# Kernel tuning notes

Measured on AMD Instinct MI355X. Metric: run time of the kernel, lower is better.

The kernel has to match this reference:

```python
import jax, jax.numpy as jnp
import numpy as np

B, T, D = 2, 1024, 2048
H = 16
NOPE, ROPE = 128, 64
QKD = NOPE + ROPE          # 192
QLORA, KVLORA = 1536, 512
VHD = 128
INTER = 8192
EPS = 1e-6
# NOTE: faithful to source: softscale = qk_head_dim * -0.5 (a large negative
# multiplier, NOT qk_head_dim ** -0.5). We reproduce the exact math.
SOFTSCALE = QKD * -0.5


def rmsnorm(x, w):
    return x * jax.lax.rsqrt(jnp.mean(jnp.square(x), axis=-1, keepdims=True) + EPS) * w


def apply_rope(x, cos, sin):
    # x: [B, T, h, rd] with rd even; cos/sin: [T, rd//2]
    x2 = x.reshape(x.shape[:-1] + (-1, 2))
    x0, x1 = x2[..., 0], x2[..., 1]
    c = cos[None, :, None, :]
    s = sin[None, :, None, :]
    r0 = x0 * c - x1 * s
    r1 = x0 * s + x1 * c
    return jnp.stack([r0, r1], axis=-1).reshape(x.shape)


def setup_inputs() -> dict:
    key = jax.random.key(0)
    ks = jax.random.split(key, 12)

    def w(k, o, i):
        return jax.random.normal(k, (o, i), jnp.float32) * 0.02

    x = jax.random.normal(ks[0], (B, T, D), jnp.float32)
    # RoPE angle tables for the rope sub-dim
    inv_freq = 1.0 / (10000.0 ** (jnp.arange(0, ROPE, 2, dtype=jnp.float32) / ROPE))
    ang = jnp.arange(T, dtype=jnp.float32)[:, None] * inv_freq[None, :]  # [T, ROPE//2]
    # causal additive mask [T, T]
    mask = jnp.where(jnp.tril(jnp.ones((T, T), bool)), 0.0, -1e9).astype(jnp.float32)
    return {
        "x": x,
        "mask": mask,
        "freqs_cos": jnp.cos(ang),
        "freqs_sin": jnp.sin(ang),
        "attn_norm_w": jnp.ones((D,), jnp.float32),
        "wq_a": w(ks[1], QLORA, D),
        "q_norm_w": jnp.ones((QLORA,), jnp.float32),
        "wq_b": w(ks[2], H * QKD, QLORA),
        "wkv_a": w(ks[3], KVLORA + ROPE, D),
        "kv_norm_w": jnp.ones((KVLORA,), jnp.float32),
        "wkv_b": w(ks[4], H * (NOPE + VHD), KVLORA),
        "wo": w(ks[5], D, H * VHD),
        "ffn_norm_w": jnp.ones((D,), jnp.float32),
        "w1": w(ks[6], INTER, D),
        "w2": w(ks[7], D, INTER),
        "w3": w(ks[8], INTER, D),
    }


def reference(x, mask, freqs_cos, freqs_sin, attn_norm_w, wq_a, q_norm_w, wq_b,
              wkv_a, kv_norm_w, wkv_b, wo, ffn_norm_w, w1, w2, w3):
    b, t, d = x.shape
    # --- MLA attention sub-block (pre-norm + residual) ---
    h = rmsnorm(x, attn_norm_w)
    # low-rank query: wq_b(q_norm(wq_a(h)))
    q = rmsnorm(h @ wq_a.T, q_norm_w) @ wq_b.T          # [b, t, H*QKD]
    q = q.reshape(b, t, H, QKD)
    q_nope, q_pe = q[..., :NOPE], q[..., NOPE:]
    q_pe = apply_rope(q_pe, freqs_cos, freqs_sin)
    # low-rank kv + decoupled rope key
    kv_all = h @ wkv_a.T                                 # [b, t, KVLORA+ROPE]
    kv_lat, k_pe = kv_all[..., :KVLORA], kv_all[..., KVLORA:]
    k_pe = apply_rope(k_pe[:, :, None, :], freqs_cos, freqs_sin)  # [b, t, 1, ROPE]
    kv = rmsnorm(kv_lat, kv_norm_w) @ wkv_b.T            # [b, t, H*(NOPE+VHD)]
    kv = kv.reshape(b, t, H, NOPE + VHD)
    k_nope, v = kv[..., :NOPE], kv[..., NOPE:]
    qf = jnp.concatenate([q_nope, q_pe], axis=-1)        # [b, t, H, QKD]
    kf = jnp.concatenate([k_nope, jnp.broadcast_to(k_pe, (b, t, H, ROPE))], axis=-1)
    scores = jnp.einsum('bshd,bthd->bsht', qf, kf) * SOFTSCALE
    scores = scores + mask[:, None, :]                   # mask over (s, 1, t)
    attn = jax.nn.softmax(scores.astype(jnp.float32), axis=-1).astype(x.dtype)
    y = jnp.einsum('bsht,bthd->bshd', attn, v).reshape(b, t, H * VHD)
    x = x + y @ wo.T
    # --- MLP sub-block (pre-norm + residual), SwiGLU ---
    h2 = rmsnorm(x, ffn_norm_w)
    out = x + (jax.nn.silu(h2 @ w1.T) * (h2 @ w3.T)) @ w2.T
    return out
```

## Files before the change

kernel.cpp:

```cpp
#include <hip/hip_runtime.h>
#include <hip/hip_bf16.h>
#include <cstddef>


#define TT 1024
#define DD 2048
#define QBLK 64
#define KVB 32

using bf16 = __hip_bfloat16;
typedef __attribute__((ext_vector_type(8))) short short8;
typedef __attribute__((ext_vector_type(8))) unsigned short ushort8v;
typedef __attribute__((ext_vector_type(4))) float f32x4;

__device__ __forceinline__ float us2f(unsigned short u) {
    return __uint_as_float(((unsigned int)u) << 16);
}
__device__ __forceinline__ float ldf(const void* p, size_t i, int isbf) {
    return isbf ? us2f(((const unsigned short*)p)[i]) : ((const float*)p)[i];
}
__device__ __forceinline__ unsigned short f2bf(float f) {
    __hip_bfloat16 b = __float2bfloat16(f);
    return *reinterpret_cast<unsigned short*>(&b);
}
// ... 58 lines not shown
            for (int u = 0; u < 8; ++u) {
                const float v = s[u];
                th[u] = f2bf(v);
                tl[u] = f2bf(v - us2f(th[u]));
            }
        }
        *(ushort8v*)(dh + i) = *(const ushort8v*)th;
        *(ushort8v*)(dl + i) = *(const ushort8v*)tl;
    }
}

template <int S, int HASR>
__global__ __launch_bounds__(256) void combine_k(
    const float* __restrict__ p, const float* __restrict__ R,
    float* __restrict__ out, int n4)
{
    const int stride = gridDim.x * 256;
    const float4* pp = (const float4*)p;
    for (int i = blockIdx.x * 256 + threadIdx.x; i < n4; i += stride) {
        float4 o = pp[i];
#pragma unroll
        for (int s = 1; s < S; ++s) {
            const float4 b4 = pp[(size_t)s * n4 + i];
            o.x += b4.x; o.y += b4.y; o.z += b4.z; o.w += b4.w;
        }
        if (HASR) {
            const float4 r4 = ((const float4*)R)[i];
            o.x += r4.x; o.y += r4.y; o.z += r4.z; o.w += r4.w;
        }
        ((float4*)out)[i] = o;
    }
}

__global__ __launch_bounds__(256) void rmsnorm_hl_k(
    const float* __restrict__ in, const void* __restrict__ w,
    unsigned short* __restrict__ oh, unsigned short* __restrict__ ol,
    int L, int istride, const int* __restrict__ flag)
{
    const int isbf = *flag;
    const int m = blockIdx.x, tid = threadIdx.x;
    const float* row = in + (size_t)m * istride;
    float ss = 0.f;
    for (int i = tid; i < L; i += 256) { float v = row[i]; ss += v * v; }
    __shared__ float red[256];
    red[tid] = ss; __syncthreads();
    for (int s = 128; s > 0; s >>= 1) {
        if (tid < s) red[tid] += red[tid + s];
        __syncthreads();
    }
    const float scale = 1.0f / sqrtf(red[0] / (float)L + 1e-6f);
    unsigned short* hrow = oh + (size_t)m * L;
    unsigned short* lrow = ol + (size_t)m * L;
    for (int i = tid; i < L; i += 256) {
        const float v = row[i] * scale * ldf(w, i, isbf);
        const unsigned short hi = f2bf(v);
        hrow[i] = hi;
        lrow[i] = f2bf(v - us2f(hi));
    }
}

__global__ __launch_bounds__(256) void rmsnorm_bf_k(
    const float* __restrict__ in, const void* __restrict__ w,
    unsigned short* __restrict__ out, int L,
    const int* __restrict__ flag)
{
    const int isbf = *flag;
    const int m = blockIdx.x, tid = threadIdx.x;
    const float* row = in + (size_t)m * L;
    float ss = 0.f;
    for (int i = tid; i < L; i += 256) { float v = row[i]; ss += v * v; }
    __shared__ float red[256];
    red[tid] = ss; __syncthreads();
    for (int s = 128; s > 0; s >>= 1) {
        if (tid < s) red[tid] += red[tid + s];
        __syncthreads();
    }
    const float scale = 1.0f / sqrtf(red[0] / (float)L + 1e-6f);
    unsigned short* orow = out + (size_t)m * L;
    for (int i = tid; i < L; i += 256)
        orow[i] = f2bf(row[i] * scale * ldf(w, i, isbf));
}

__global__ __launch_bounds__(256) void rmsnorm_x_hl_k(
    const void* __restrict__ x, size_t eoff, const void* __restrict__ w,
    unsigned short* __restrict__ hh, unsigned short* __restrict__ hl,
    float* __restrict__ xf, const int* __restrict__ flag)
{
    const int isbf = *flag;
    const int m = blockIdx.x, tid = threadIdx.x;
    const size_t base = eoff + (size_t)m * DD;
    float* xrow = xf + (size_t)m * DD;
    float ss = 0.f;
    float vals[8];
    for (int i = 0; i < 8; ++i) {
        float v = ldf(x, base + tid + 256 * i, isbf);
        vals[i] = v; ss += v * v;
        xrow[tid + 256 * i] = v;
    }
    __shared__ float red[256];
    red[tid] = ss; __syncthreads();
    for (int s = 128; s > 0; s >>= 1) {
        if (tid < s) red[tid] += red[tid + s];
        __syncthreads();
    }
    const float scale = 1.0f / sqrtf(red[0] / (float)DD + 1e-6f);
    unsigned short* hrow = hh + (size_t)m * DD;
    unsigned short* lrow = hl + (size_t)m * DD;
    for (int i = 0; i < 8; ++i) {
        const float v = vals[i] * scale * ldf(w, tid + 256 * i, isbf);
        const unsigned short hi = f2bf(v);
        hrow[tid + 256 * i] = hi;
        lrow[tid + 256 * i] = f2bf(v - us2f(hi));
    }
}

__global__ __launch_bounds__(256) void gemm_mfma3_k(
    const unsigned short* __restrict__ Ah, const unsigned short* __restrict__ Al,
    const void* __restrict__ Wv, const unsigned short* __restrict__ Wlo,
    float* __restrict__ C, int N, int K, int klen,
    int presplit, const int* __restrict__ flag)
{
    __shared__ __align__(16) unsigned short lds[20480];
    const int tid = threadIdx.x;
    const int lane = tid & 63;
    const int wave = tid >> 6;
    const int wm = (wave >> 1) << 6, wn = (wave & 1) << 6;
    const int bm = blockIdx.y << 7, bn = blockIdx.x << 7;
    const int k0 = blockIdx.z * klen;
    const size_t zoff = (size_t)blockIdx.z * 1024 * N;
    const int frow = lane & 15;
    const int fk = (lane >> 4) << 3;
    const int kend = k0 + klen;

    f32x4 acc[4][4] = {};

    if (presplit) {
        unsigned short* Lah = lds;
        unsigned short* Lal = lds + 4096;
        unsigned short* Lwh = lds + 8192;
        unsigned short* Lwl = lds + 12288;
        const unsigned short* Whp = (const unsigned short*)Wv;
        const int lrow = lane >> 2;
        const int sp8 = ((lane & 3) ^ (lrow & 3)) << 3;
        const int rA0 = wave * 32 + lrow;
        const int rA1 = wave * 32 + 16 + lrow;
        const int wr0 = (bn + rA0 < N) ? bn + rA0 : N - 1;
        const int wr1 = (bn + rA1 < N) ? bn + rA1 : N - 1;
        const size_t gA0 = (size_t)(bm + rA0) * K + sp8;
        const size_t gA1 = (size_t)(bm + rA1) * K + sp8;
        const size_t gW0 = (size_t)wr0 * K + sp8;
        const size_t gW1 = (size_t)wr1 * K + sp8;
        unsigned short* d0 = lds + wave * 1024;
        const int xa = ((fk >> 3) ^ (frow & 3)) << 3;

        for (int kt = k0; kt < kend; kt += 32) {
            gld16(Ah + gA0 + kt, Lah + wave * 1024);
            gld16(Ah + gA1 + kt, Lah + wave * 1024 + 512);
            gld16(Al + gA0 + kt, Lal + wave * 1024);
            gld16(Al + gA1 + kt, Lal + wave * 1024 + 512);
            gld16(Whp + gW0 + kt, Lwh + wave * 1024);
            gld16(Whp + gW1 + kt, Lwh + wave * 1024 + 512);
            gld16(Wlo + gW0 + kt, Lwl + wave * 1024);
            gld16(Wlo + gW1 + kt, Lwl + wave * 1024 + 512);
            __syncthreads();

            short8 afh[4], afl[4], bfh[4], bfl[4];
#pragma unroll
            for (int i = 0; i < 4; ++i) {
                afh[i] = *(const short8*)&Lah[(wm + i * 16 + frow) * 32 + xa];
                afl[i] = *(const short8*)&Lal[(wm + i * 16 + frow) * 32 + xa];
            }
#pragma unroll
            for (int j = 0; j < 4; ++j) {
                bfh[j] = *(const short8*)&Lwh[(wn + j * 16 + frow) * 32 + xa];
                bfl[j] = *(const short8*)&Lwl[(wn + j * 16 + frow) * 32 + xa];
            }
#pragma unroll
            for (int i = 0; i < 4; ++i)
#pragma unroll
                for (int j = 0; j < 4; ++j) {
                    acc[i][j] = __builtin_amdgcn_mfma_f32_16x16x32_bf16(
                        afh[i], bfh[j], acc[i][j], 0, 0, 0);
                    acc[i][j] = __builtin_amdgcn_mfma_f32_16x16x32_bf16(
                        afh[i], bfl[j], acc[i][j], 0, 0, 0);
                    acc[i][j] = __builtin_amdgcn_mfma_f32_16x16x32_bf16(
                        afl[i], bfh[j], acc[i][j], 0, 0, 0);
                }
            __syncthreads();
        }
        (void)d0;
    } else {
        unsigned short* Ash = lds;
        unsigned short* Asl = lds + 5120;
        unsigned short* Wsh = lds + 10240;
        unsigned short* Wsl = lds + 15360;
        const int isbf = *flag;
        const int srow = tid >> 1, scol = (tid & 1) << 4;
        const unsigned short* Ahld = Ah + (size_t)(bm + srow) * K + scol;
        const unsigned short* Alld = Al + (size_t)(bm + srow) * K + scol;
        const int wrow = bn + srow;
        const size_t wldbase = (size_t)((wrow < N) ? wrow : (N - 1)) * K + scol;
        unsigned short* Ahdst = &Ash[srow * 40 + scol];
        unsigned short* Aldst = &Asl[srow * 40 + scol];
        unsigned short* Whdst = &Wsh[srow * 40 + scol];
        unsigned short* Wldst = &Wsl[srow * 40 + scol];
        for (int kt = k0; kt < kend; kt += 32) {
            ushort8v a0h = *(const ushort8v*)(Ahld + kt);
            ushort8v a1h = *(const ushort8v*)(Ahld + kt + 8);
            ushort8v a0l = *(const ushort8v*)(Alld + kt);
            ushort8v a1l = *(const ushort8v*)(Alld + kt + 8);
            ushort8v w0h, w1h, w0l, w1l;
            if (isbf) {
                const unsigned short* Wp = (const unsigned short*)Wv + wldbase + kt;
                w0h = *(const ushort8v*)(Wp);
                w1h = *(const ushort8v*)(Wp + 8);
                w0l = w0h ^ w0h;
                w1l = w0l;
            } else {
                const float* Wp = (const float*)Wv + wldbase + kt;
                unsigned short th[16], tl[16];
#pragma unroll
                for (int t4 = 0; t4 < 4; ++t4) {
                    float4 f = *(const float4*)(Wp + 4 * t4);
                    float fv[4] = {f.x, f.y, f.z, f.w};
#pragma unroll
                    for (int u = 0; u < 4; ++u) {
                        const unsigned short hi = f2bf(fv[u]);
                        th[4 * t4 + u] = hi;
                        tl[4 * t4 + u] = f2bf(fv[u] - us2f(hi));
                    }
                }
                w0h = *(ushort8v*)&th[0]; w1h = *(ushort8v*)&th[8];
                w0l = *(ushort8v*)&tl[0]; w1l = *(ushort8v*)&tl[8];
            }
            __syncthreads();
            *(ushort8v*)Ahdst = a0h; *(ushort8v*)(Ahdst + 8) = a1h;
            *(ushort8v*)Aldst = a0l; *(ushort8v*)(Aldst + 8) = a1l;
            *(ushort8v*)Whdst = w0h; *(ushort8v*)(Whdst + 8) = w1h;
            *(ushort8v*)Wldst = w0l; *(ushort8v*)(Wldst + 8) = w1l;
            __syncthreads();

            short8 afh[4], afl[4], bfh[4], bfl[4];
#pragma unroll
            for (int i = 0; i < 4; ++i) {
                afh[i] = *(const short8*)&Ash[(wm + i * 16 + frow) * 40 + fk];
                afl[i] = *(const short8*)&Asl[(wm + i * 16 + frow) * 40 + fk];
            }
#pragma unroll
            for (int j = 0; j < 4; ++j) {
                bfh[j] = *(const short8*)&Wsh[(wn + j * 16 + frow) * 40 + fk];
                bfl[j] = *(const short8*)&Wsl[(wn + j * 16 + frow) * 40 + fk];
            }
#pragma unroll
            for (int i = 0; i < 4; ++i)
#pragma unroll
                for (int j = 0; j < 4; ++j) {
                    acc[i][j] = __builtin_amdgcn_mfma_f32_16x16x32_bf16(
                        afh[i], bfh[j], acc[i][j], 0, 0, 0);
                    acc[i][j] = __builtin_amdgcn_mfma_f32_16x16x32_bf16(
                        afh[i], bfl[j], acc[i][j], 0, 0, 0);
                    acc[i][j] = __builtin_amdgcn_mfma_f32_16x16x32_bf16(
                        afl[i], bfh[j], acc[i][j], 0, 0, 0);
                }
        }
    }

#pragma unroll
    for (int i = 0; i < 4; ++i) {
        const int r0 = bm + wm + i * 16 + ((lane >> 4) << 2);
#pragma unroll
        for (int j = 0; j < 4; ++j) {
            const int c = bn + wn + j * 16 + (lane & 15);
            if (c < N) {
#pragma unroll
                for (int g = 0; g < 4; ++g)
                    C[zoff + (size_t)(r0 + g) * N + c] = acc[i][j][g];
            }
        }
    }
}

template <int EPI>
__global__ __launch_bounds__(256) void gemm_mfma_k(
    const unsigned short* __restrict__ A, const void* __restrict__ Wv,
    const float* __restrict__ R, void* __restrict__ outp,
    int N, int K, int klen, int wready, const int* __restrict__ flag)
{
    __shared__ __align__(16) unsigned short lds[10240];
    const int tid = threadIdx.x;
    const int lane = tid & 63;
    const int wave = tid >> 6;
    const int wm = (wave >> 1) << 6, wn = (wave & 1) << 6;
    const int bm = blockIdx.y << 7, bn = blockIdx.x << 7;
    const int k0 = blockIdx.z * klen;
    const size_t zoff = (size_t)blockIdx.z * 1024 * N;
    const int frow = lane & 15;
    const int fk = (lane >> 4) << 3;
    const int kend = k0 + klen;

    f32x4 acc[4][4] = {};

    if (wready) {
        unsigned short* As = lds;
        unsigned short* Ws = lds + 4096;
        const unsigned short* Wp = (const unsigned short*)Wv;
        const int lrow = lane >> 2;
        const int sp8 = ((lane & 3) ^ (lrow & 3)) << 3;
        const int rA0 = wave * 32 + lrow;
        const int rA1 = wave * 32 + 16 + lrow;
        const size_t gA0 = (size_t)(bm + rA0) * K + sp8;
        const size_t gA1 = (size_t)(bm + rA1) * K + sp8;
        const size_t gW0 = (size_t)(bn + rA0) * K + sp8;
        const size_t gW1 = (size_t)(bn + rA1) * K + sp8;
        const int xa = ((fk >> 3) ^ (frow & 3)) << 3;

        for (int kt = k0; kt < kend; kt += 32) {
            gld16(A + gA0 + kt, As + wave * 1024);
            gld16(A + gA1 + kt, As + wave * 1024 + 512);
            gld16(Wp + gW0 + kt, Ws + wave * 1024);
            gld16(Wp + gW1 + kt, Ws + wave * 1024 + 512);
            __syncthreads();

            short8 af[4], bfr[4];
#pragma unroll
            for (int i = 0; i < 4; ++i)
                af[i] = *(const short8*)&As[(wm + i * 16 + frow) * 32 + xa];
#pragma unroll
            for (int j = 0; j < 4; ++j)
                bfr[j] = *(const short8*)&Ws[(wn + j * 16 + frow) * 32 + xa];
#pragma unroll
            for (int i = 0; i < 4; ++i)
#pragma unroll
                for (int j = 0; j < 4; ++j)
                    acc[i][j] = __builtin_amdgcn_mfma_f32_16x16x32_bf16(
                        af[i], bfr[j], acc[i][j], 0, 0, 0);
            __syncthreads();
        }
    } else {
        unsigned short* As = lds;
        unsigned short* Ws = lds + 5120;
        const int isbf = *flag;
        const int srow = tid >> 1, scol = (tid & 1) << 4;
        const unsigned short* Ald = A + (size_t)(bm + srow) * K + scol;
        const size_t wldbase = (size_t)(bn + srow) * K + scol;
        unsigned short* Adst = &As[srow * 40 + scol];
        unsigned short* Wdst = &Ws[srow * 40 + scol];
        for (int kt = k0; kt < kend; kt += 32) {
            ushort8v a0 = *(const ushort8v*)(Ald + kt);
            ushort8v a1 = *(const ushort8v*)(Ald + kt + 8);
            ushort8v w0, w1;
            if (isbf) {
                const unsigned short* Wpp = (const unsigned short*)Wv + wldbase + kt;
                w0 = *(const ushort8v*)(Wpp);
                w1 = *(const ushort8v*)(Wpp + 8);
            } else {
                const float* Wpp = (const float*)Wv + wldbase + kt;
                float4 f0 = *(const float4*)(Wpp);
                float4 f1 = *(const float4*)(Wpp + 4);
                float4 f2 = *(const float4*)(Wpp + 8);
                float4 f3 = *(const float4*)(Wpp + 12);
                unsigned short wt[16];
                wt[0] = f2bf(f0.x); wt[1] = f2bf(f0.y); wt[2]  = f2bf(f0.z); wt[3]  = f2bf(f0.w);
                wt[4] = f2bf(f1.x); wt[5] = f2bf(f1.y); wt[6]  = f2bf(f1.z); wt[7]  = f2bf(f1.w);
                wt[8] = f2bf(f2.x); wt[9] = f2bf(f2.y); wt[10] = f2bf(f2.z); wt[11] = f2bf(f2.w);
                wt[12] = f2bf(f3.x); wt[13] = f2bf(f3.y); wt[14] = f2bf(f3.z); wt[15] = f2bf(f3.w);
                w0 = *(const ushort8v*)&wt[0];
                w1 = *(const ushort8v*)&wt[8];
            }
            __syncthreads();
            *(ushort8v*)Adst = a0; *(ushort8v*)(Adst + 8) = a1;
            *(ushort8v*)Wdst = w0; *(ushort8v*)(Wdst + 8) = w1;
            __syncthreads();

            short8 af[4], bfr[4];
#pragma unroll
            for (int i = 0; i < 4; ++i)
                af[i] = *(const short8*)&As[(wm + i * 16 + frow) * 40 + fk];
#pragma unroll
// ... 98 lines not shown
        unsigned short* As = lds;
        unsigned short* Ws1 = lds + 5120;
        unsigned short* Ws3 = lds + 10240;
        const int isbf = *flag;
        const int srow = tid >> 1, scol = (tid & 1) << 4;
        const unsigned short* Ald = A + (size_t)(bm + srow) * K + scol;
        const size_t wldbase = (size_t)(bn + srow) * K + scol;
        unsigned short* Adst = &As[srow * 40 + scol];
        unsigned short* W1dst = &Ws1[srow * 40 + scol];
        unsigned short* W3dst = &Ws3[srow * 40 + scol];
        for (int kt = 0; kt < K; kt += 32) {
            ushort8v a0 = *(const ushort8v*)(Ald + kt);
            ushort8v a1 = *(const ushort8v*)(Ald + kt + 8);
            ushort8v w10, w11, w30, w31;
            if (isbf) {
                const unsigned short* W1p = (const unsigned short*)W1v + wldbase + kt;
                const unsigned short* W3p = (const unsigned short*)W3v + wldbase + kt;
                w10 = *(const ushort8v*)(W1p); w11 = *(const ushort8v*)(W1p + 8);
                w30 = *(const ushort8v*)(W3p); w31 = *(const ushort8v*)(W3p + 8);
            } else {
                const float* W1p = (const float*)W1v + wldbase + kt;
                const float* W3p = (const float*)W3v + wldbase + kt;
                unsigned short t1[16], t3[16];
#pragma unroll
                for (int t4 = 0; t4 < 4; ++t4) {
                    float4 f1 = *(const float4*)(W1p + 4 * t4);
                    float4 f3 = *(const float4*)(W3p + 4 * t4);
                    float v1[4] = {f1.x, f1.y, f1.z, f1.w};
                    float v3[4] = {f3.x, f3.y, f3.z, f3.w};
#pragma unroll
                    for (int u = 0; u < 4; ++u) {
                        t1[4 * t4 + u] = f2bf(v1[u]);
                        t3[4 * t4 + u] = f2bf(v3[u]);
                    }
                }
                w10 = *(ushort8v*)&t1[0]; w11 = *(ushort8v*)&t1[8];
                w30 = *(ushort8v*)&t3[0]; w31 = *(ushort8v*)&t3[8];
            }
            __syncthreads();
            *(ushort8v*)Adst = a0; *(ushort8v*)(Adst + 8) = a1;
            *(ushort8v*)W1dst = w10; *(ushort8v*)(W1dst + 8) = w11;
            *(ushort8v*)W3dst = w30; *(ushort8v*)(W3dst + 8) = w31;
            __syncthreads();

            short8 af[4], b1[4], b3[4];
#pragma unroll
            for (int i = 0; i < 4; ++i)
                af[i] = *(const short8*)&As[(wm + i * 16 + frow) * 40 + fk];
#pragma unroll
            for (int j = 0; j < 4; ++j) {
                b1[j] = *(const short8*)&Ws1[(wn + j * 16 + frow) * 40 + fk];
                b3[j] = *(const short8*)&Ws3[(wn + j * 16 + frow) * 40 + fk];
            }
#pragma unroll
            for (int i = 0; i < 4; ++i)
#pragma unroll
                for (int j = 0; j < 4; ++j) {
                    acc1[i][j] = __builtin_amdgcn_mfma_f32_16x16x32_bf16(
                        af[i], b1[j], acc1[i][j], 0, 0, 0);
                    acc3[i][j] = __builtin_amdgcn_mfma_f32_16x16x32_bf16(
                        af[i], b3[j], acc3[i][j], 0, 0, 0);
                }
        }
    }

#pragma unroll
    for (int i = 0; i < 4; ++i) {
        const int r0 = bm + wm + i * 16 + ((lane >> 4) << 2);
#pragma unroll
        for (int j = 0; j < 4; ++j) {
            const int c = bn + wn + j * 16 + (lane & 15);
#pragma unroll
            for (int g = 0; g < 4; ++g) {
                const float gv = acc1[i][j][g];
                const float sg = 1.0f / (1.0f + __expf(-gv));
                outp[(size_t)(r0 + g) * N + c] = f2bf(gv * sg * acc3[i][j][g]);
            }
        }
    }
}

__global__ __launch_bounds__(256) void rope_k(
    float* __restrict__ qb, float* __restrict__ kva,
    const void* __restrict__ fc, const void* __restrict__ fs,
    const int* __restrict__ flag)
{
    const int isbf = *flag;
    const int t = blockIdx.x;
    const int tid = threadIdx.x;
    __shared__ float c[32], s[32];
    if (tid < 32) {
        c[tid] = ldf(fc, t * 32 + tid, isbf);
        s[tid] = ldf(fs, t * 32 + tid, isbf);
    }
    __syncthreads();
    for (int p = tid; p < 512; p += 256) {
        const int h = p >> 5, i = p & 31;
        float* base = qb + (size_t)t * 3072 + h * 192 + 128 + 2 * i;
        const float x0 = base[0], x1 = base[1];
        base[0] = x0 * c[i] - x1 * s[i];
        base[1] = x0 * s[i] + x1 * c[i];
    }
    if (tid < 32) {
        float* base = kva + (size_t)t * 576 + 512 + 2 * tid;
        const float x0 = base[0], x1 = base[1];
        base[0] = x0 * c[tid] - x1 * s[tid];
        base[1] = x0 * s[tid] + x1 * c[tid];
    }
}

__global__ __launch_bounds__(256) void kvprep_k(
    const float* __restrict__ kvb,
    const float* __restrict__ kva,
    unsigned short* __restrict__ kh, unsigned short* __restrict__ kl,
    unsigned short* __restrict__ vt)
{
    const int tt = blockIdx.x, h = blockIdx.y;
    const int tid = threadIdx.x;
    const int tbase = tt * 64;
    for (int i = tid; i < 64 * 192; i += 256) {
        const int t = i / 192, k = i % 192;
        const float v = (k < 128)
            ? kvb[(size_t)(tbase + t) * 4096 + h * 256 + k]
            : kva[(size_t)(tbase + t) * 576 + 512 + (k - 128)];
        const unsigned short hi = f2bf(v);
        const size_t o = ((size_t)h * 1024 + tbase + t) * 192 + k;
        kh[o] = hi;
        kl[o] = f2bf(v - us2f(hi));
    }
    __shared__ unsigned short Vl[128][72];
    for (int i = tid; i < 64 * 128; i += 256) {
        const int t = i >> 7, d = i & 127;
        Vl[d][t] = f2bf(kvb[(size_t)(tbase + t) * 4096 + h * 256 + 128 + d]);
    }
    __syncthreads();
    for (int i = tid; i < 128 * 64; i += 256) {
        const int d = i >> 6, t = i & 63;
        vt[((size_t)h * 128 + d) * 1024 + tbase + t] = Vl[d][t];
    }
}

__global__ __launch_bounds__(256) void attn_mfma_k(
    const float* __restrict__ qb,
    const unsigned short* __restrict__ kh,
    const unsigned short* __restrict__ kl,
    const unsigned short* __restrict__ vt,
    float* __restrict__ opart)
{
    const int qt = blockIdx.x, h = blockIdx.y, z = blockIdx.z;
    const int s0 = qt * QBLK;
    const int tid = threadIdx.x;
    const int lane = tid & 63, wave = tid >> 6;
    const int frow = lane & 15;
    const int fk8 = (lane >> 4) << 3;
    const int g4 = (lane >> 4) << 2;

    __shared__ __align__(16) unsigned short Ksh[KVB][200];
    __shared__ __align__(16) unsigned short Ksl[KVB][200];
    __shared__ __align__(16) unsigned short Vs[128][40];
    __shared__ __align__(16) unsigned short Ps[4][16][40];

    const int wrow0 = s0 + wave * 16;
    short8 qhf[6], qlf[6];
    {
        const float* qrow = qb + (size_t)(wrow0 + frow) * 3072 + h * 192 + fk8;
#pragma unroll
        for (int ks = 0; ks < 6; ++ks) {
            float4 f0 = *(const float4*)(qrow + ks * 32);
            float4 f1 = *(const float4*)(qrow + ks * 32 + 4);
            float fv[8] = {f0.x, f0.y, f0.z, f0.w, f1.x, f1.y, f1.z, f1.w};
            unsigned short th[8], tl[8];
#pragma unroll
            for (int u = 0; u < 8; ++u) {
                th[u] = f2bf(fv[u]);
                tl[u] = f2bf(fv[u] - us2f(th[u]));
            }
            qhf[ks] = *(short8*)th;
            qlf[ks] = *(short8*)tl;
        }
    }

    f32x4 O[8] = {};
    float m_run[4] = {-1e30f, -1e30f, -1e30f, -1e30f};
    float l_run[4] = {};

    const int t_beg = z * (qt + 1);
    const int t_end = t_beg + (qt + 1);
    for (int tt = t_beg; tt < t_end; ++tt) {
        const int t0 = tt * KVB;
        __syncthreads();
        for (int i = tid; i < KVB * 24; i += 256) {
            const int r = i / 24, c = (i % 24) * 8;
            const size_t gof = ((size_t)h * 1024 + t0 + r) * 192 + c;
            *(ushort8v*)&Ksh[r][c] = *(const ushort8v*)(kh + gof);
            *(ushort8v*)&Ksl[r][c] = *(const ushort8v*)(kl + gof);
        }
        for (int i = tid; i < 128 * 4; i += 256) {
            const int d = i >> 2, c = (i & 3) * 8;
            *(ushort8v*)&Vs[d][c] =
                *(const ushort8v*)(vt + ((size_t)h * 128 + d) * 1024 + t0 + c);
        }
        __syncthreads();

        const bool active = (t0 <= wrow0 + 15);
        if (active) {
            f32x4 s[2] = {};
#pragma unroll
            for (int j = 0; j < 2; ++j) {
                const unsigned short* kb = &Ksh[j * 16 + frow][fk8];
                const unsigned short* lb = &Ksl[j * 16 + frow][fk8];
#pragma unroll
                for (int ks = 0; ks < 6; ++ks) {
                    short8 bh = *(const short8*)(kb + ks * 32);
                    short8 bl = *(const short8*)(lb + ks * 32);
                    s[j] = __builtin_amdgcn_mfma_f32_16x16x32_bf16(qhf[ks], bh, s[j], 0, 0, 0);
                    s[j] = __builtin_amdgcn_mfma_f32_16x16x32_bf16(qhf[ks], bl, s[j], 0, 0, 0);
                    s[j] = __builtin_amdgcn_mfma_f32_16x16x32_bf16(qlf[ks], bh, s[j], 0, 0, 0);
                }
            }
            const bool edge = (t0 + KVB - 1 > wrow0);
            float sv[2][4];
#pragma unroll
            for (int j = 0; j < 2; ++j)
#pragma unroll
                for (int g = 0; g < 4; ++g) {
                    float v = s[j][g] * -96.0f;
                    if (edge) {
                        const int col = t0 + j * 16 + frow;
                        const int row = wrow0 + g4 + g;
                        if (col > row) v = -1e30f;
                    }
                    sv[j][g] = v;
                }
            float alpha[4];
#pragma unroll
            for (int g = 0; g < 4; ++g) {
                float mt = fmaxf(sv[0][g], sv[1][g]);
                mt = fmaxf(mt, __shfl_xor(mt, 1));
                mt = fmaxf(mt, __shfl_xor(mt, 2));
                mt = fmaxf(mt, __shfl_xor(mt, 4));
                mt = fmaxf(mt, __shfl_xor(mt, 8));
                const float mn = fmaxf(m_run[g], mt);
                alpha[g] = __expf(m_run[g] - mn);
                m_run[g] = mn;
                const float p0 = __expf(sv[0][g] - mn);
                const float p1 = __expf(sv[1][g] - mn);
                sv[0][g] = p0; sv[1][g] = p1;
                float ps = p0 + p1;
                ps += __shfl_xor(ps, 1);
                ps += __shfl_xor(ps, 2);
                ps += __shfl_xor(ps, 4);
                ps += __shfl_xor(ps, 8);
                l_run[g] = l_run[g] * alpha[g] + ps;
            }
#pragma unroll
            for (int jt = 0; jt < 8; ++jt)
#pragma unroll
                for (int g = 0; g < 4; ++g)
                    O[jt][g] *= alpha[g];
#pragma unroll
            for (int j = 0; j < 2; ++j)
#pragma unroll
                for (int g = 0; g < 4; ++g)
                    Ps[wave][g4 + g][j * 16 + frow] = f2bf(sv[j][g]);
        }
        __syncthreads();
        if (active) {
            short8 pa = *(const short8*)&Ps[wave][frow][fk8];
#pragma unroll
            for (int jt = 0; jt < 8; ++jt) {
                short8 vb = *(const short8*)&Vs[jt * 16 + frow][fk8];
                O[jt] = __builtin_amdgcn_mfma_f32_16x16x32_bf16(pa, vb, O[jt], 0, 0, 0);
            }
        }
    }

#pragma unroll
    for (int g = 0; g < 4; ++g) {
        const int row = wrow0 + g4 + g;
        float* rec = opart + (((size_t)z * 1024 + row) * 16 + h) * 66;
        unsigned short* ob = (unsigned short*)rec;
#pragma unroll
        for (int jt = 0; jt < 8; ++jt)
            ob[jt * 16 + frow] = f2bf(O[jt][g]);
        if ((lane & 15) == 0) { rec[64] = m_run[g]; rec[65] = l_run[g]; }
    }
}

__global__ __launch_bounds__(256) void attn_merge_k(
    const float* __restrict__ opart, unsigned short* __restrict__ y)
{
    const int r = blockIdx.x;
    for (int i = threadIdx.x; i < 2048; i += 256) {
        const int h = i >> 7, d = i & 127;
        const float* r0 = opart + (((size_t)r) * 16 + h) * 66;
        const float* r1 = opart + (((size_t)1024 + r) * 16 + h) * 66;
        const float m0 = r0[64], l0 = r0[65];
        const float m1 = r1[64], l1 = r1[65];
        const float mm = fmaxf(m0, m1);
        const float a0 = __expf(m0 - mm), a1 = __expf(m1 - mm);
        const float denom = l0 * a0 + l1 * a1;
        const float o0 = us2f(((const unsigned short*)r0)[d]);
        const float o1 = us2f(((const unsigned short*)r1)[d]);
        y[(size_t)r * 2048 + h * 128 + d] = f2bf((o0 * a0 + o1 * a1) / denom);
    }
}

extern "C" void kernel_launch(void* const* d_in, const int* in_sizes, int n_in,
                              void* d_out, int out_size, void* d_ws, size_t ws_size,
                              hipStream_t stream) {
    (void)in_sizes; (void)n_in; (void)out_size;
    const void* x       = d_in[0];
    const void* fcos    = d_in[2];
    const void* fsin    = d_in[3];
    const void* attn_nw = d_in[4];
    const void* wq_a    = d_in[5];
    const void* q_nw    = d_in[6];
    const void* wq_b    = d_in[7];
    const void* wkv_a   = d_in[8];
    const void* kv_nw   = d_in[9];
    const void* wkv_b   = d_in[10];
    const void* wo      = d_in[11];
    const void* ffn_nw  = d_in[12];
    const void* w1      = d_in[13];
    const void* w2      = d_in[14];
    const void* w3      = d_in[15];

    int* flag = (int*)d_ws;
    float* a  = (float*)d_ws + 64;
    const size_t M1 = 1048576;
    float* xf  = a;
    unsigned short* hh = (unsigned short*)(a + 2 * M1);
    unsigned short* hl = (unsigned short*)(a + 3 * M1);
    float* qa  = a + 4 * M1;
    float* kva = a + 4 * M1;
    unsigned short* kvnh = (unsigned short*)(a + 4 * M1 + 655360);
    unsigned short* kvnl = (unsigned short*)(a + 4 * M1 + 655360 + 262144);
    unsigned short* qah = (unsigned short*)(a + 5 * M1 + 524288);
    unsigned short* qal = (unsigned short*)(a + 6 * M1 + 262144);
    float* qb  = a + 7 * M1;
    float* kvb = a + 10 * M1;
    unsigned short* kh = (unsigned short*)(a + 2 * M1);
    unsigned short* kl = (unsigned short*)(a + 5 * M1 + 524288);
    unsigned short* vt = (unsigned short*)(a + 14 * M1);
    unsigned short* yb = (unsigned short*)(a + 3 * M1 + 524288);
    unsigned short* hb  = (unsigned short*)(a + 2 * M1);
    unsigned short* gb2 = (unsigned short*)(a + 12 * M1);
    float* x2  = xf;
    float* sp  = a + 10 * M1;
    float* fpo = a + 5 * M1;
    float* fp2 = a + 2 * M1;
    float* opart = a + 10 * M1;
    unsigned short* wo_b  = (unsigned short*)(a + 16 * M1);
    unsigned short* w1_b  = (unsigned short*)(a + 18 * M1);
    unsigned short* w3_b  = (unsigned short*)(a + 26 * M1);
    unsigned short* w2_b  = (unsigned short*)(a + 34 * M1);
    unsigned short* wqa_h = (unsigned short*)(a + 42 * M1);
    unsigned short* wqa_l = wqa_h + 3145728u;
    unsigned short* wqb_h = (unsigned short*)(a + 45 * M1);
    unsigned short* wqb_l = wqb_h + 4718592u;
    unsigned short* wkva_h = (unsigned short*)(a + 49 * M1 + 524288);
    unsigned short* wkva_l = wkva_h + 1179648u;
    unsigned short* wkvb_h = (unsigned short*)(a + 50 * M1 + 655360);
    unsigned short* wkvb_l = wkvb_h + 2097152u;
    const size_t NEED = 256 + (size_t)(52 * M1 + 655360) * 4;
    const int prep = (ws_size >= NEED) ? 1 : 0;

    detect_k<<<1, 64, 0, stream>>>(x, flag);

    if (prep) {
        cvt_bf_k<<<1024, 256, 0, stream>>>(wo, wo_b, (size_t)2048 * 2048, flag);
        cvt_bf_k<<<2048, 256, 0, stream>>>(w1, w1_b, (size_t)8192 * 2048, flag);
        cvt_bf_k<<<2048, 256, 0, stream>>>(w3, w3_b, (size_t)8192 * 2048, flag);
        cvt_bf_k<<<2048, 256, 0, stream>>>(w2, w2_b, (size_t)2048 * 8192, flag);
        cvt_hl_k<<<1024, 256, 0, stream>>>(wq_a, wqa_h, wqa_l, (size_t)1536 * 2048, flag);
        cvt_hl_k<<<1024, 256, 0, stream>>>(wq_b, wqb_h, wqb_l, (size_t)3072 * 1536, flag);
        cvt_hl_k<<<512, 256, 0, stream>>>(wkv_a, wkva_h, wkva_l, (size_t)576 * 2048, flag);
        cvt_hl_k<<<1024, 256, 0, stream>>>(wkv_b, wkvb_h, wkvb_l, (size_t)4096 * 512, flag);
    }
    const void* Wqa = prep ? (const void*)wqa_h : wq_a;
    const void* Wqb = prep ? (const void*)wqb_h : wq_b;
    const void* Wkva = prep ? (const void*)wkva_h : wkv_a;
    const void* Wkvb = prep ? (const void*)wkvb_h : wkv_b;
    const unsigned short* WqaL = prep ? wqa_l : nullptr;
    const unsigned short* WqbL = prep ? wqb_l : nullptr;
    const unsigned short* WkvaL = prep ? wkva_l : nullptr;
    const unsigned short* WkvbL = prep ? wkvb_l : nullptr;
    const void* WoP = prep ? (const void*)wo_b : wo;
    const void* W1P = prep ? (const void*)w1_b : w1;
    const void* W3P = prep ? (const void*)w3_b : w3;
    const void* W2P = prep ? (const void*)w2_b : w2;

    for (int b = 0; b < 2; ++b) {
        const size_t eoff = (size_t)b * TT * DD;
        float* outb = (float*)d_out + eoff;

        rmsnorm_x_hl_k<<<TT, 256, 0, stream>>>(x, eoff, attn_nw, hh, hl, xf, flag);
        gemm_mfma3_k<<<dim3(12, 8, 4), 256, 0, stream>>>(hh, hl, Wqa, WqaL, sp, 1536, 2048, 512, prep, flag);
        combine_k<4, 0><<<1024, 256, 0, stream>>>(sp, nullptr, qa, 393216);
        rmsnorm_hl_k<<<TT, 256, 0, stream>>>(qa, q_nw, qah, qal, 1536, 1536, flag);
        gemm_mfma3_k<<<dim3(24, 8, 2), 256, 0, stream>>>(qah, qal, Wqb, WqbL, sp, 3072, 1536, 768, prep, flag);
        combine_k<2, 0><<<1024, 256, 0, stream>>>(sp, nullptr, qb, 786432);
        gemm_mfma3_k<<<dim3(5, 8, 8), 256, 0, stream>>>(hh, hl, Wkva, WkvaL, sp, 576, 2048, 256, prep, flag);
        combine_k<8, 0><<<1024, 256, 0, stream>>>(sp, nullptr, kva, 147456);
        rmsnorm_hl_k<<<TT, 256, 0, stream>>>(kva, kv_nw, kvnh, kvnl, 512, 576, flag);
        rope_k<<<TT, 256, 0, stream>>>(qb, kva, fcos, fsin, flag);
        gemm_mfma3_k<<<dim3(32, 8, 1), 256, 0, stream>>>(kvnh, kvnl, Wkvb, WkvbL, kvb, 4096, 512, 512, prep, flag);
        kvprep_k<<<dim3(16, 16), 256, 0, stream>>>(kvb, kva, kh, kl, vt);
        attn_mfma_k<<<dim3(TT / QBLK, 16, 2), 256, 0, stream>>>(qb, kh, kl, vt, opart);
        attn_merge_k<<<TT, 256, 0, stream>>>(opart, yb);

        gemm_mfma_k<0><<<dim3(16, 8, 4), 256, 0, stream>>>(yb, WoP, nullptr, fpo, 2048, 2048, 512, prep, flag);
        combine_k<4, 1><<<1024, 256, 0, stream>>>(fpo, xf, x2, 524288);
        rmsnorm_bf_k<<<TT, 256, 0, stream>>>(x2, ffn_nw, hb, 2048, flag);
        gemm_swiglu_k<<<dim3(64, 8), 256, 0, stream>>>(hb, W1P, W3P, gb2, 8192, 2048, prep, flag);
        gemm_mfma_k<0><<<dim3(16, 8, 4), 256, 0, stream>>>(gb2, W2P, nullptr, fp2, 2048, 8192, 2048, prep, flag);
        combine_k<4, 1><<<1024, 256, 0, stream>>>(fp2, x2, outb, 524288);
    }
}
```

Measured before the change: 1.325 ms.

## Process both batches in one launch sequence and fuse KV prep into GEMM epilogue

```diff
diff --git a/kernel.cpp b/kernel.cpp
--- a/kernel.cpp
+++ b/kernel.cpp
@@ -164,13 +164,13 @@
 }
 
 __global__ __launch_bounds__(256) void rmsnorm_x_hl_k(
-    const void* __restrict__ x, size_t eoff, const void* __restrict__ w,
+    const void* __restrict__ x, const void* __restrict__ w,
     unsigned short* __restrict__ hh, unsigned short* __restrict__ hl,
     float* __restrict__ xf, const int* __restrict__ flag)
 {
     const int isbf = *flag;
     const int m = blockIdx.x, tid = threadIdx.x;
-    const size_t base = eoff + (size_t)m * DD;
+    const size_t base = (size_t)m * DD;
     float* xrow = xf + (size_t)m * DD;
     float ss = 0.f;
     float vals[8];
@@ -200,7 +200,9 @@
     const unsigned short* __restrict__ Ah, const unsigned short* __restrict__ Al,
     const void* __restrict__ Wv, const unsigned short* __restrict__ Wlo,
     float* __restrict__ C, int N, int K, int klen,
-    int presplit, const int* __restrict__ flag)
+    int presplit, const int* __restrict__ flag,
+    int epikv, unsigned short* __restrict__ okh,
+    unsigned short* __restrict__ okl, unsigned short* __restrict__ ovt)
 {
     __shared__ __align__(16) unsigned short lds[20480];
     const int tid = threadIdx.x;
@@ -209,7 +211,7 @@
     const int wm = (wave >> 1) << 6, wn = (wave & 1) << 6;
     const int bm = blockIdx.y << 7, bn = blockIdx.x << 7;
     const int k0 = blockIdx.z * klen;
-    const size_t zoff = (size_t)blockIdx.z * 1024 * N;
+    const size_t zoff = (size_t)blockIdx.z * 2048 * N;
     const int frow = lane & 15;
     const int fk = (lane >> 4) << 3;
     const int kend = k0 + klen;
@@ -232,7 +234,6 @@
         const size_t gA1 = (size_t)(bm + rA1) * K + sp8;
         const size_t gW0 = (size_t)wr0 * K + sp8;
         const size_t gW1 = (size_t)wr1 * K + sp8;
-        unsigned short* d0 = lds + wave * 1024;
         const int xa = ((fk >> 3) ^ (frow & 3)) << 3;
 
         for (int kt = k0; kt < kend; kt += 32) {
@@ -270,7 +271,6 @@
                 }
             __syncthreads();
         }
-        (void)d0;
     } else {
         unsigned short* Ash = lds;
         unsigned short* Asl = lds + 5120;
@@ -347,16 +347,41 @@
         }
     }
 
-#pragma unroll
-    for (int i = 0; i < 4; ++i) {
-        const int r0 = bm + wm + i * 16 + ((lane >> 4) << 2);
-#pragma unroll
-        for (int j = 0; j < 4; ++j) {
-            const int c = bn + wn + j * 16 + (lane & 15);
-            if (c < N) {
-#pragma unroll
-                for (int g = 0; g < 4; ++g)
-                    C[zoff + (size_t)(r0 + g) * N + c] = acc[i][j][g];
+    if (!epikv) {
+#pragma unroll
+        for (int i = 0; i < 4; ++i) {
+            const int r0 = bm + wm + i * 16 + ((lane >> 4) << 2);
+#pragma unroll
+            for (int j = 0; j < 4; ++j) {
+                const int c = bn + wn + j * 16 + (lane & 15);
+                if (c < N) {
+#pragma unroll
+                    for (int g = 0; g < 4; ++g)
+                        C[zoff + (size_t)(r0 + g) * N + c] = acc[i][j][g];
+                }
+            }
+        }
+    } else {
+#pragma unroll
+        for (int i = 0; i < 4; ++i) {
+            const int r0 = bm + wm + i * 16 + ((lane >> 4) << 2);
+#pragma unroll
+            for (int j = 0; j < 4; ++j) {
+                const int c = bn + wn + j * 16 + (lane & 15);
+                const int h = c >> 8, cc = c & 255;
+#pragma unroll
+                for (int g = 0; g < 4; ++g) {
+                    const int t = r0 + g;
+                    const float v = acc[i][j][g];
+                    if (cc < 128) {
+                        const size_t o = ((size_t)h * 2048 + t) * 192 + cc;
+                        const unsigned short hi = f2bf(v);
+                        okh[o] = hi;
+                        okl[o] = f2bf(v - us2f(hi));
+                    } else {
+                        ovt[((size_t)h * 128 + (cc - 128)) * 2048 + t] = f2bf(v);
+                    }
+                }
             }
         }
     }
@@ -375,7 +400,7 @@
     const int wm = (wave >> 1) << 6, wn = (wave & 1) << 6;
     const int bm = blockIdx.y << 7, bn = blockIdx.x << 7;
     const int k0 = blockIdx.z * klen;
-    const size_t zoff = (size_t)blockIdx.z * 1024 * N;
+    const size_t zoff = (size_t)blockIdx.z * 2048 * N;
     const int frow = lane & 15;
     const int fk = (lane >> 4) << 3;
     const int kend = k0 + klen;
@@ -640,11 +665,13 @@
 
 __global__ __launch_bounds__(256) void rope_k(
     float* __restrict__ qb, float* __restrict__ kva,
+    unsigned short* __restrict__ kh, unsigned short* __restrict__ kl,
     const void* __restrict__ fc, const void* __restrict__ fs,
     const int* __restrict__ flag)
 {
     const int isbf = *flag;
-    const int t = blockIdx.x;
+    const int r = blockIdx.x;
+    const int t = r & 1023;
     const int tid = threadIdx.x;
     __shared__ float c[32], s[32];
     if (tid < 32) {
@@ -654,47 +681,26 @@
     __syncthreads();
     for (int p = tid; p < 512; p += 256) {
         const int h = p >> 5, i = p & 31;
-        float* base = qb + (size_t)t * 3072 + h * 192 + 128 + 2 * i;
+        float* base = qb + (size_t)r * 3072 + h * 192 + 128 + 2 * i;
         const float x0 = base[0], x1 = base[1];
         base[0] = x0 * c[i] - x1 * s[i];
         base[1] = x0 * s[i] + x1 * c[i];
     }
     if (tid < 32) {
-        float* base = kva + (size_t)t * 576 + 512 + 2 * tid;
+        float* base = kva + (size_t)r * 576 + 512 + 2 * tid;
         const float x0 = base[0], x1 = base[1];
-        base[0] = x0 * c[tid] - x1 * s[tid];
-        base[1] = x0 * s[tid] + x1 * c[tid];
-    }
-}
-
-__global__ __launch_bounds__(256) void kvprep_k(
-    const float* __restrict__ kvb,
-    const float* __restrict__ kva,
-    unsigned short* __restrict__ kh, unsigned short* __restrict__ kl,
-    unsigned short* __restrict__ vt)
-{
-    const int tt = blockIdx.x, h = blockIdx.y;
-    const int tid = threadIdx.x;
-    const int tbase = tt * 64;
-    for (int i = tid; i < 64 * 192; i += 256) {
-        const int t = i / 192, k = i % 192;
-        const float v = (k < 128)
-            ? kvb[(size_t)(tbase + t) * 4096 + h * 256 + k]
-            : kva[(size_t)(tbase + t) * 576 + 512 + (k - 128)];
-        const unsigned short hi = f2bf(v);
-        const size_t o = ((size_t)h * 1024 + tbase + t) * 192 + k;
-        kh[o] = hi;
-        kl[o] = f2bf(v - us2f(hi));
-    }
-    __shared__ unsigned short Vl[128][72];
-    for (int i = tid; i < 64 * 128; i += 256) {
-        const int t = i >> 7, d = i & 127;
-        Vl[d][t] = f2bf(kvb[(size_t)(tbase + t) * 4096 + h * 256 + 128 + d]);
-    }
-    __syncthreads();
-    for (int i = tid; i < 128 * 64; i += 256) {
-        const int d = i >> 6, t = i & 63;
-        vt[((size_t)h * 128 + d) * 1024 + tbase + t] = Vl[d][t];
+        const float r0 = x0 * c[tid] - x1 * s[tid];
+        const float r1 = x0 * s[tid] + x1 * c[tid];
+        base[0] = r0;
+        base[1] = r1;
+        const unsigned short h0 = f2bf(r0), h1 = f2bf(r1);
+        const unsigned short l0 = f2bf(r0 - us2f(h0)), l1 = f2bf(r1 - us2f(h1));
+#pragma unroll
+        for (int h = 0; h < 16; ++h) {
+            const size_t o = ((size_t)h * 2048 + r) * 192 + 128 + 2 * tid;
+            kh[o] = h0; kh[o + 1] = h1;
+            kl[o] = l0; kl[o + 1] = l1;
+        }
     }
 }
 
@@ -705,8 +711,10 @@
     const unsigned short* __restrict__ vt,
     float* __restrict__ opart)
 {
-    const int qt = blockIdx.x, h = blockIdx.y, z = blockIdx.z;
-    const int s0 = qt * QBLK;
+    const int qtg = blockIdx.x, h = blockIdx.y, z = blockIdx.z;
+    const int batch = qtg >> 4;
+    const int lqt = qtg & 15;
+    const int tb = batch << 10;
     const int tid = threadIdx.x;
     const int lane = tid & 63, wave = tid >> 6;
     const int frow = lane & 15;
@@ -718,10 +726,11 @@
     __shared__ __align__(16) unsigned short Vs[128][40];
     __shared__ __align__(16) unsigned short Ps[4][16][40];
 
-    const int wrow0 = s0 + wave * 16;
+    const int wrow0l = lqt * QBLK + wave * 16;
+    const int wrow0g = qtg * QBLK + wave * 16;
     short8 qhf[6], qlf[6];
     {
-        const float* qrow = qb + (size_t)(wrow0 + frow) * 3072 + h * 192 + fk8;
+        const float* qrow = qb + (size_t)(wrow0g + frow) * 3072 + h * 192 + fk8;
 #pragma unroll
         for (int ks = 0; ks < 6; ++ks) {
             float4 f0 = *(const float4*)(qrow + ks * 32);
@@ -742,25 +751,26 @@
     float m_run[4] = {-1e30f, -1e30f, -1e30f, -1e30f};
     float l_run[4] = {};
 
-    const int t_beg = z * (qt + 1);
-    const int t_end = t_beg + (qt + 1);
+    const int t_beg = z * (lqt + 1);
+    const int t_end = t_beg + (lqt + 1);
     for (int tt = t_beg; tt < t_end; ++tt) {
-        const int t0 = tt * KVB;
+        const int t0l = tt * KVB;
+        const int t0g = tb + t0l;
         __syncthreads();
         for (int i = tid; i < KVB * 24; i += 256) {
             const int r = i / 24, c = (i % 24) * 8;
-            const size_t gof = ((size_t)h * 1024 + t0 + r) * 192 + c;
+            const size_t gof = ((size_t)h * 2048 + t0g + r) * 192 + c;
             *(ushort8v*)&Ksh[r][c] = *(const ushort8v*)(kh + gof);
             *(ushort8v*)&Ksl[r][c] = *(const ushort8v*)(kl + gof);
         }
         for (int i = tid; i < 128 * 4; i += 256) {
             const int d = i >> 2, c = (i & 3) * 8;
             *(ushort8v*)&Vs[d][c] =
-                *(const ushort8v*)(vt + ((size_t)h * 128 + d) * 1024 + t0 + c);
+                *(const ushort8v*)(vt + ((size_t)h * 128 + d) * 2048 + t0g + c);
         }
         __syncthreads();
 
-        const bool active = (t0 <= wrow0 + 15);
+        const bool active = (t0l <= wrow0l + 15);
         if (active) {
             f32x4 s[2] = {};
 #pragma unroll
@@ -776,7 +786,7 @@
                     s[j] = __builtin_amdgcn_mfma_f32_16x16x32_bf16(qlf[ks], bh, s[j], 0, 0, 0);
                 }
             }
-            const bool edge = (t0 + KVB - 1 > wrow0);
+            const bool edge = (t0l + KVB - 1 > wrow0l);
             float sv[2][4];
 #pragma unroll
             for (int j = 0; j < 2; ++j)
@@ -784,8 +794,8 @@
                 for (int g = 0; g < 4; ++g) {
                     float v = s[j][g] * -96.0f;
                     if (edge) {
-                        const int col = t0 + j * 16 + frow;
-                        const int row = wrow0 + g4 + g;
+                        const int col = t0l + j * 16 + frow;
+                        const int row = wrow0l + g4 + g;
                         if (col > row) v = -1e30f;
                     }
                     sv[j][g] = v;
@@ -835,8 +845,8 @@
 
 #pragma unroll
     for (int g = 0; g < 4; ++g) {
-        const int row = wrow0 + g4 + g;
-        float* rec = opart + (((size_t)z * 1024 + row) * 16 + h) * 66;
+        const int row = wrow0g + g4 + g;
+        float* rec = opart + (((size_t)z * 2048 + row) * 16 + h) * 66;
         unsigned short* ob = (unsigned short*)rec;
 #pragma unroll
         for (int jt = 0; jt < 8; ++jt)
@@ -852,7 +862,7 @@
     for (int i = threadIdx.x; i < 2048; i += 256) {
         const int h = i >> 7, d = i & 127;
         const float* r0 = opart + (((size_t)r) * 16 + h) * 66;
-        const float* r1 = opart + (((size_t)1024 + r) * 16 + h) * 66;
+        const float* r1 = opart + (((size_t)2048 + r) * 16 + h) * 66;
         const float m0 = r0[64], l0 = r0[65];
         const float m1 = r1[64], l1 = r1[65];
         const float mm = fmaxf(m0, m1);
@@ -888,40 +898,39 @@
     float* a  = (float*)d_ws + 64;
     const size_t M1 = 1048576;
     float* xf  = a;
-    unsigned short* hh = (unsigned short*)(a + 2 * M1);
-    unsigned short* hl = (unsigned short*)(a + 3 * M1);
-    float* qa  = a + 4 * M1;
-    float* kva = a + 4 * M1;
-    unsigned short* kvnh = (unsigned short*)(a + 4 * M1 + 655360);
-    unsigned short* kvnl = (unsigned short*)(a + 4 * M1 + 655360 + 262144);
-    unsigned short* qah = (unsigned short*)(a + 5 * M1 + 524288);
-    unsigned short* qal = (unsigned short*)(a + 6 * M1 + 262144);
-    float* qb  = a + 7 * M1;
-    float* kvb = a + 10 * M1;
-    unsigned short* kh = (unsigned short*)(a + 2 * M1);
-    unsigned short* kl = (unsigned short*)(a + 5 * M1 + 524288);
-    unsigned short* vt = (unsigned short*)(a + 14 * M1);
-    unsigned short* yb = (unsigned short*)(a + 3 * M1 + 524288);
-    unsigned short* hb  = (unsigned short*)(a + 2 * M1);
-    unsigned short* gb2 = (unsigned short*)(a + 12 * M1);
+    unsigned short* hh = (unsigned short*)(a + 4 * M1);
+    unsigned short* hl = (unsigned short*)(a + 6 * M1);
+    float* sp  = a + 8 * M1;
+    float* qa  = a + 14 * M1;
+    unsigned short* qah = (unsigned short*)(a + 8 * M1);
+    unsigned short* qal = (unsigned short*)(a + 9 * M1 + 524288);
+    float* qb  = a + 17 * M1;
+    float* kva = a + 12 * M1 + 524288;
+    unsigned short* kvnh = (unsigned short*)(a + 13 * M1 + 655360);
+    unsigned short* kvnl = kvnh + 1048576;
+    unsigned short* kh = (unsigned short*)(a + 4 * M1);
+    unsigned short* kl = (unsigned short*)(a + 7 * M1);
+    unsigned short* vt = (unsigned short*)(a + 10 * M1);
+    float* opart = a + 12 * M1 + 524288;
+    unsigned short* yb = (unsigned short*)(a + 4 * M1);
+    float* fpo = a + 6 * M1;
+    unsigned short* hb  = (unsigned short*)(a + 4 * M1);
+    unsigned short* gb2 = (unsigned short*)(a + 6 * M1);
+    float* fp2 = a + 14 * M1;
     float* x2  = xf;
-    float* sp  = a + 10 * M1;
-    float* fpo = a + 5 * M1;
-    float* fp2 = a + 2 * M1;
-    float* opart = a + 10 * M1;
-    unsigned short* wo_b  = (unsigned short*)(a + 16 * M1);
-    unsigned short* w1_b  = (unsigned short*)(a + 18 * M1);
-    unsigned short* w3_b  = (unsigned short*)(a + 26 * M1);
-    unsigned short* w2_b  = (unsigned short*)(a + 34 * M1);
-    unsigned short* wqa_h = (unsigned short*)(a + 42 * M1);
+    unsigned short* wo_b  = (unsigned short*)(a + 23 * M1);
+    unsigned short* w1_b  = (unsigned short*)(a + 25 * M1);
+    unsigned short* w3_b  = (unsigned short*)(a + 33 * M1);
+    unsigned short* w2_b  = (unsigned short*)(a + 41 * M1);
+    unsigned short* wqa_h = (unsigned short*)(a + 49 * M1);
     unsigned short* wqa_l = wqa_h + 3145728u;
-    unsigned short* wqb_h = (unsigned short*)(a + 45 * M1);
+    unsigned short* wqb_h = (unsigned short*)(a + 52 * M1);
     unsigned short* wqb_l = wqb_h + 4718592u;
-    unsigned short* wkva_h = (unsigned short*)(a + 49 * M1 + 524288);
+    unsigned short* wkva_h = (unsigned short*)(a + 56 * M1 + 524288);
     unsigned short* wkva_l = wkva_h + 1179648u;
-    unsigned short* wkvb_h = (unsigned short*)(a + 50 * M1 + 655360);
+    unsigned short* wkvb_h = (unsigned short*)(a + 57 * M1 + 655360);
     unsigned short* wkvb_l = wkvb_h + 2097152u;
-    const size_t NEED = 256 + (size_t)(52 * M1 + 655360) * 4;
+    const size_t NEED = 256 + (size_t)(59 * M1 + 655360) * 4;
     const int prep = (ws_size >= NEED) ? 1 : 0;
 
     detect_k<<<1, 64, 0, stream>>>(x, flag);
@@ -949,30 +958,23 @@
     const void* W3P = prep ? (const void*)w3_b : w3;
     const void* W2P = prep ? (const void*)w2_b : w2;
 
-    for (int b = 0; b < 2; ++b) {
-        const size_t eoff = (size_t)b * TT * DD;
-        float* outb = (float*)d_out + eoff;
-
-        rmsnorm_x_hl_k<<<TT, 256, 0, stream>>>(x, eoff, attn_nw, hh, hl, xf, flag);
-        gemm_mfma3_k<<<dim3(12, 8, 4), 256, 0, stream>>>(hh, hl, Wqa, WqaL, sp, 1536, 2048, 512, prep, flag);
-        combine_k<4, 0><<<1024, 256, 0, stream>>>(sp, nullptr, qa, 393216);
-        rmsnorm_hl_k<<<TT, 256, 0, stream>>>(qa, q_nw, qah, qal, 1536, 1536, flag);
-        gemm_mfma3_k<<<dim3(24, 8, 2), 256, 0, stream>>>(qah, qal, Wqb, WqbL, sp, 3072, 1536, 768, prep, flag);
-        combine_k<2, 0><<<1024, 256, 0, stream>>>(sp, nullptr, qb, 786432);
-        gemm_mfma3_k<<<dim3(5, 8, 8), 256, 0, stream>>>(hh, hl, Wkva, WkvaL, sp, 576, 2048, 256, prep, flag);
-        combine_k<8, 0><<<1024, 256, 0, stream>>>(sp, nullptr, kva, 147456);
-        rmsnorm_hl_k<<<TT, 256, 0, stream>>>(kva, kv_nw, kvnh, kvnl, 512, 576, flag);
-        rope_k<<<TT, 256, 0, stream>>>(qb, kva, fcos, fsin, flag);
-        gemm_mfma3_k<<<dim3(32, 8, 1), 256, 0, stream>>>(kvnh, kvnl, Wkvb, WkvbL, kvb, 4096, 512, 512, prep, flag);
-        kvprep_k<<<dim3(16, 16), 256, 0, stream>>>(kvb, kva, kh, kl, vt);
-        attn_mfma_k<<<dim3(TT / QBLK, 16, 2), 256, 0, stream>>>(qb, kh, kl, vt, opart);
-        attn_merge_k<<<TT, 256, 0, stream>>>(opart, yb);
-
-        gemm_mfma_k<0><<<dim3(16, 8, 4), 256, 0, stream>>>(yb, WoP, nullptr, fpo, 2048, 2048, 512, prep, flag);
-        combine_k<4, 1><<<1024, 256, 0, stream>>>(fpo, xf, x2, 524288);
-        rmsnorm_bf_k<<<TT, 256, 0, stream>>>(x2, ffn_nw, hb, 2048, flag);
-        gemm_swiglu_k<<<dim3(64, 8), 256, 0, stream>>>(hb, W1P, W3P, gb2, 8192, 2048, prep, flag);
-        gemm_mfma_k<0><<<dim3(16, 8, 4), 256, 0, stream>>>(gb2, W2P, nullptr, fp2, 2048, 8192, 2048, prep, flag);
-        combine_k<4, 1><<<1024, 256, 0, stream>>>(fp2, x2, outb, 524288);
-    }
-}
+    rmsnorm_x_hl_k<<<2048, 256, 0, stream>>>(x, attn_nw, hh, hl, xf, flag);
+    gemm_mfma3_k<<<dim3(12, 16, 2), 256, 0, stream>>>(hh, hl, Wqa, WqaL, sp, 1536, 2048, 1024, prep, flag, 0, nullptr, nullptr, nullptr);
+    combine_k<2, 0><<<2048, 256, 0, stream>>>(sp, nullptr, qa, 786432);
+    rmsnorm_hl_k<<<2048, 256, 0, stream>>>(qa, q_nw, qah, qal, 1536, 1536, flag);
+    gemm_mfma3_k<<<dim3(24, 16, 1), 256, 0, stream>>>(qah, qal, Wqb, WqbL, qb, 3072, 1536, 1536, prep, flag, 0, nullptr, nullptr, nullptr);
+    gemm_mfma3_k<<<dim3(5, 16, 4), 256, 0, stream>>>(hh, hl, Wkva, WkvaL, sp, 576, 2048, 512, prep, flag, 0, nullptr, nullptr, nullptr);
+    combine_k<4, 0><<<2048, 256, 0, stream>>>(sp, nullptr, kva, 294912);
+    rmsnorm_hl_k<<<2048, 256, 0, stream>>>(kva, kv_nw, kvnh, kvnl, 512, 576, flag);
+    rope_k<<<2048, 256, 0, stream>>>(qb, kva, kh, kl, fcos, fsin, flag);
+    gemm_mfma3_k<<<dim3(32, 16, 1), 256, 0, stream>>>(kvnh, kvnl, Wkvb, WkvbL, nullptr, 4096, 512, 512, prep, flag, 1, kh, kl, vt);
+    attn_mfma_k<<<dim3(32, 16, 2), 256, 0, stream>>>(qb, kh, kl, vt, opart);
+    attn_merge_k<<<2048, 256, 0, stream>>>(opart, yb);
+
+    gemm_mfma_k<0><<<dim3(16, 16, 2), 256, 0, stream>>>(yb, WoP, nullptr, fpo, 2048, 2048, 1024, prep, flag);
+    combine_k<2, 1><<<2048, 256, 0, stream>>>(fpo, xf, x2, 1048576);
+    rmsnorm_bf_k<<<2048, 256, 0, stream>>>(x2, ffn_nw, hb, 2048, flag);
+    gemm_swiglu_k<<<dim3(64, 16), 256, 0, stream>>>(hb, W1P, W3P, gb2, 8192, 2048, prep, flag);
+    gemm_mfma_k<0><<<dim3(16, 16, 2), 256, 0, stream>>>(gb2, W2P, nullptr, fp2, 2048, 8192, 4096, prep, flag);
+    combine_k<2, 1><<<2048, 256, 0, stream>>>(fp2, x2, (float*)d_out, 1048576);
+}
```

Measured after the change: 1.181 ms. 1.12x faster.
